# Kernel optimization log

Hardware: AMD Instinct MI355X
Metric: run time of the kernel (lower is better)

## Reference

```python
import jax, jax.numpy as jnp
import numpy as np

B, C, H, W = 4, 2048, 32, 32
HID, A, G = 512, 9, 20
SCALE = 32.0
POS_T, NEG_T = 0.7, 0.3
W_CONF, W_REG = 1.0, 5.0
EPS = 1e-8


def _anchor_base():
    # gen_anc_centers + gen_anc_base: centers at (i+0.5); anc_w=scale, anc_h=scale*ratio; clipped to feature-map extent
    scales = jnp.array([2.0, 4.0, 6.0])
    ratios = jnp.array([0.5, 1.0, 1.5])
    aw = jnp.repeat(scales, 3)                       # [A]
    ah = (scales[:, None] * ratios[None, :]).reshape(-1)
    xc = (jnp.arange(W) + 0.5)[None, :, None]        # [1,W,1]
    yc = (jnp.arange(H) + 0.5)[:, None, None]        # [H,1,1]
    x1 = jnp.clip(xc - aw / 2, 0.0, W)
    y1 = jnp.clip(yc - ah / 2, 0.0, H)
    x2 = jnp.clip(xc + aw / 2, 0.0, W)
    y2 = jnp.clip(yc + ah / 2, 0.0, H)
    anc = jnp.stack(jnp.broadcast_arrays(x1, y1, x2, y2), axis=-1)  # [H,W,A,4]
    return anc.reshape(-1, 4)                        # [N,4], N = H*W*A


def _conv(x, w, b):
    y = jax.lax.conv_general_dilated(x, w, (1, 1), 'SAME',
                                     dimension_numbers=('NCHW', 'OIHW', 'NCHW'))
    return y + b[None, :, None, None]


def setup_inputs():
    key = jax.random.key(0)
    ks = jax.random.split(key, 8)
    feature_map = jax.random.normal(ks[0], (B, C, H, W), jnp.float32)
    # valid GT boxes in pixel coords of a 1024x1024 image
    ctr = jax.random.uniform(ks[1], (B, G, 2), minval=0.15, maxval=0.85) * 1024.0
    wh = jax.random.uniform(ks[2], (B, G, 2), minval=0.05, maxval=0.30) * 1024.0
    gt_bboxes = jnp.clip(jnp.concatenate([ctr - wh / 2, ctr + wh / 2], -1), 0.0, 1024.0)
    gt_classes = jax.random.randint(ks[3], (B, G), 1, 21)
    f1 = 1.0 / np.sqrt(C * 9)
    f2 = 1.0 / np.sqrt(HID)
    conv1_w = jax.random.uniform(ks[4], (HID, C, 3, 3), jnp.float32, -f1, f1)
    conv1_b = jnp.zeros((HID,), jnp.float32)
    conf_w = jax.random.uniform(ks[5], (A, HID, 1, 1), jnp.float32, -f2, f2)
    conf_b = jnp.zeros((A,), jnp.float32)
    reg_w = jax.random.uniform(ks[6], (A * 4, HID, 1, 1), jnp.float32, -f2, f2)
    reg_b = jnp.zeros((A * 4,), jnp.float32)
    return {"feature_map": feature_map, "gt_bboxes": gt_bboxes, "gt_classes": gt_classes,
            "conv1_w": conv1_w, "conv1_b": conv1_b, "conf_w": conf_w, "conf_b": conf_b,
            "reg_w": reg_w, "reg_b": reg_b}


def reference(feature_map, gt_bboxes, gt_classes, conv1_w, conv1_b, conf_w, conf_b, reg_w, reg_b):
    # ProposalModule (dropout = eval identity)
    hid = jax.nn.relu(_conv(feature_map, conv1_w, conv1_b))
    conf = _conv(hid, conf_w, conf_b).transpose(0, 2, 3, 1).reshape(B, -1)       # [B,N]
    offs = _conv(hid, reg_w, reg_b).transpose(0, 2, 3, 1).reshape(B, -1, 4)      # [B,N,4]

    anc = _anchor_base()                              # [N,4]
    gt = gt_bboxes / SCALE                            # project_bboxes p2a

    # IoU [B,N,G]
    lt = jnp.maximum(anc[None, :, None, :2], gt[:, None, :, :2])
    rb = jnp.minimum(anc[None, :, None, 2:], gt[:, None, :, 2:])
    inter = jnp.clip(rb - lt, 0.0).prod(-1)
    area_a = (anc[:, 2] - anc[:, 0]) * (anc[:, 3] - anc[:, 1])
    area_g = (gt[..., 2] - gt[..., 0]) * (gt[..., 3] - gt[..., 1])
    iou = inter / (area_a[None, :, None] + area_g[:, None, :] - inter + EPS)

    # positive: IoU > pos_thresh OR best anchor for each GT; negative: max IoU < neg_thresh
    max_per_gt = iou.max(axis=1, keepdims=True)
    pos = ((iou > POS_T) | ((iou == max_per_gt) & (max_per_gt > EPS))).any(-1)    # [B,N]
    max_per_anc = iou.max(-1)
    gi = iou.argmax(-1)                               # assigned GT per anchor
    neg = (max_per_anc < NEG_T) & (~pos)

    assigned = jnp.take_along_axis(gt, jnp.broadcast_to(gi[:, :, None], gi.shape + (4,)), axis=1)

    acx = (anc[:, 0] + anc[:, 2]) / 2; acy = (anc[:, 1] + anc[:, 3]) / 2
    aw_ = anc[:, 2] - anc[:, 0];       ah_ = anc[:, 3] - anc[:, 1]
    gcx = (assigned[..., 0] + assigned[..., 2]) / 2; gcy = (assigned[..., 1] + assigned[..., 3]) / 2
    gw = assigned[..., 2] - assigned[..., 0];        gh = assigned[..., 3] - assigned[..., 1]
    gt_off = jnp.stack([(gcx - acx) / (aw_ + EPS), (gcy - acy) / (ah_ + EPS),
                        jnp.log((gw + EPS) / (aw_ + EPS)), jnp.log((gh + EPS) / (ah_ + EPS))], -1)

    posf = pos.astype(conf.dtype)
    negf = neg.astype(conf.dtype)
    # BCE-with-logits, reduction='sum' / batch_size (pos target 1, neg target 0)
    cls_loss = ((jax.nn.softplus(-conf) * posf).sum() + (jax.nn.softplus(conf) * negf).sum()) / B
    d = offs - gt_off
    sl1 = jnp.where(jnp.abs(d) < 1.0, 0.5 * d * d, jnp.abs(d) - 0.5)
    reg_loss = (sl1 * posf[..., None]).sum() / B
    total = W_CONF * cls_loss + W_REG * reg_loss

    # generate_proposals from positive anchors + predicted offsets (mask instead of gather for jit)
    pcx = acx + offs[..., 0] * aw_; pcy = acy + offs[..., 1] * ah_
    pw = aw_ * jnp.exp(offs[..., 2]); ph = ah_ * jnp.exp(offs[..., 3])
    proposals = jnp.stack([pcx - pw / 2, pcy - ph / 2, pcx + pw / 2, pcy + ph / 2], -1)
    proposals = proposals * posf[..., None]
    return total, proposals, pos
```

## Files before the change

kernel.cpp:

```cpp
#include <hip/hip_runtime.h>


typedef __bf16 bf16x8 __attribute__((ext_vector_type(8)));
typedef float floatx4 __attribute__((ext_vector_type(4)));

#define NB 4
#define NC 2048
#define NH 32
#define NW 32
#define NHID 512
#define NA 9
#define NG 20
#define NANC 9216
#define NM 4096

#define OFF_XH    0ull
#define OFF_WT    18939904ull
#define OFF_WH    37814272ull
#define OFF_HB    37863424ull
#define OFF_MAXG  37863680ull
#define OFF_SUMS  37864192ull
#define OFF_CTR   37864320ull
#define OFF_HIDP  37864448ull

#define PREP_TX   4096
#define PREP_W    1024
#define PREP_WH   96
#define PREP_HALO 528
#define PREP_MAXG 80
#define PREP_NBLK (PREP_TX + PREP_W + PREP_WH + PREP_HALO + PREP_MAXG + 1)

__device__ __forceinline__ unsigned short f2bf(float f) {
  unsigned int u = __float_as_uint(f);
  u = (u + 0x7fffu + ((u >> 16) & 1u)) >> 16;
  return (unsigned short)u;
}

__device__ __forceinline__ void gload16(const void* g, void* l) {
  __builtin_amdgcn_global_load_lds(
      (const __attribute__((address_space(1))) unsigned int*)g,
      (__attribute__((address_space(3))) unsigned int*)l, 16, 0, 0);
}

__constant__ float c_aw[9] = {2.f,2.f,2.f,4.f,4.f,4.f,6.f,6.f,6.f};
__constant__ float c_ah[9] = {1.f,2.f,3.f,2.f,4.f,6.f,3.f,6.f,9.f};

struct Anc { float x1, y1, x2, y2, areaA; };
__device__ __forceinline__ Anc anc_of(int n) {
  const int a = n % 9, pix = n / 9;
  const int xi = pix & 31, yi = pix >> 5;
  const float hw = c_aw[a]*0.5f, hh = c_ah[a]*0.5f;
  const float xc = xi + 0.5f, yc = yi + 0.5f;
  Anc A;
  A.x1 = fminf(fmaxf(xc - hw, 0.f), 32.f);
  A.y1 = fminf(fmaxf(yc - hh, 0.f), 32.f);
  A.x2 = fminf(fmaxf(xc + hw, 0.f), 32.f);
  A.y2 = fminf(fmaxf(yc + hh, 0.f), 32.f);
  A.areaA = __fmul_rn(__fsub_rn(A.x2, A.x1), __fsub_rn(A.y2, A.y1));
  return A;
}
__device__ __forceinline__ float iou_one(const Anc& A, float4 gp) {
  const float gx1 = gp.x * 0.03125f, gy1 = gp.y * 0.03125f;
  const float gx2 = gp.z * 0.03125f, gy2 = gp.w * 0.03125f;
  const float dx = fmaxf(__fsub_rn(fminf(A.x2, gx2), fmaxf(A.x1, gx1)), 0.f);
  const float dy = fmaxf(__fsub_rn(fminf(A.y2, gy2), fmaxf(A.y1, gy1)), 0.f);
  const float inter = __fmul_rn(dx, dy);
  const float areaG = __fmul_rn(__fsub_rn(gx2, gx1), __fsub_rn(gy2, gy1));
  const float den = __fadd_rn(__fsub_rn(__fadd_rn(A.areaA, areaG), inter), 1e-8f);
  return __fdiv_rn(inter, den);
}

__global__ __launch_bounds__(256) void k_prep(const float* __restrict__ x,
                                              const float* __restrict__ w1,
                                              const float* __restrict__ cw, const float* __restrict__ cb,
                                              const float* __restrict__ rw, const float* __restrict__ rb,
                                              const float* __restrict__ gtb,
                                              unsigned short* __restrict__ xh,
                                              unsigned short* __restrict__ wt,
                                              unsigned short* __restrict__ wh, float* __restrict__ hb,
                                              unsigned int* __restrict__ maxg,
                                              float* __restrict__ sums, unsigned int* __restrict__ ctr) {
  __shared__ float tile[64][33];
  __shared__ unsigned short wlds[9*1024];
  __shared__ float red[4];
  const int bid = blockIdx.x;
  const int tid = threadIdx.x;

  if (bid < PREP_TX) {
    const int c0 = (bid & 31) << 6;
    const int h  = (bid >> 5) & 31;
    const int b  = bid >> 10;
    const int w = tid & 31, cl = tid >> 5;
    const float* src = x + (((size_t)b*NC + c0)*NH + h)*NW;
#pragma unroll
    for (int j = 0; j < 8; ++j) {
      const int c = cl + j*8;
      tile[c][w] = src[(size_t)c*NH*NW + w];
    }
    __syncthreads();
    unsigned short* dst = xh + ((size_t)(b*34 + h + 1)*34 + 1)*2048 + c0;
    const int w2 = tid >> 3, c8 = (tid & 7) << 3;
    unsigned int pk[4];
#pragma unroll
    for (int k = 0; k < 4; ++k) {
      const unsigned int lo = f2bf(tile[c8 + 2*k][w2]);
      const unsigned int hi = f2bf(tile[c8 + 2*k + 1][w2]);
      pk[k] = lo | (hi << 16);
    }
    *(uint4*)(dst + (size_t)w2*2048 + c8) = make_uint4(pk[0], pk[1], pk[2], pk[3]);
    return;
  }
  if (bid < PREP_TX + PREP_W) {
    const int p = bid - PREP_TX;
    const int o = p >> 1, half = p & 1;
    const int c_base = half << 10;
    const float* src = w1 + ((size_t)(o*2048 + c_base))*9;
#pragma unroll
    for (int j = 0; j < 9; ++j) {
      const int f0 = (j*256 + tid)*4;
      const float4 v = *(const float4*)(src + f0);
      const float vv[4] = {v.x, v.y, v.z, v.w};
#pragma unroll
      for (int e = 0; e < 4; ++e) {
        const int f = f0 + e;
        const int c = f/9, g = f - c*9;
        wlds[g*1024 + c] = f2bf(vv[e]);
      }
    }
    __syncthreads();
#pragma unroll
    for (int j = 0; j < 5; ++j) {
      const int idx = j*256 + tid;
      if (idx < 1152) {
        const int g = idx >> 7, off = (idx & 127) << 3;
        *(uint4*)(wt + (size_t)g*NHID*NC + o*2048 + c_base + off) =
            *(const uint4*)(wlds + g*1024 + off);
      }
    }
    return;
  }
  if (bid < PREP_TX + PREP_W + PREP_WH) {
    const int t = (bid - PREP_TX - PREP_W)*256 + tid;
    const int n = t >> 9, c = t & 511;
    float v = 0.f;
    if (n < 9) v = cw[n*512 + c];
    else if (n < 45) v = rw[(n-9)*512 + c];
    wh[t] = f2bf(v);
    if (c == 0) {
      float bv = 0.f;
      if (n < 9) bv = cb[n];
      else if (n < 45) bv = rb[n-9];
      hb[n] = bv;
    }
    return;
  }
  if (bid < PREP_TX + PREP_W + PREP_WH + PREP_HALO) {
    const int q = bid - (PREP_TX + PREP_W + PREP_WH);
    const int b = q / 132, hc = q - b*132;
    int hh, ww;
    if (hc < 34)       { hh = 0;        ww = hc; }
    else if (hc < 68)  { hh = 33;       ww = hc - 34; }
    else if (hc < 100) { hh = hc - 67;  ww = 0; }
    else               { hh = hc - 99;  ww = 33; }
    uint4* dst = (uint4*)(xh + ((size_t)((b*34 + hh)*34 + ww))*2048);
    dst[tid] = make_uint4(0u, 0u, 0u, 0u);
    return;
  }
  if (bid < PREP_TX + PREP_W + PREP_WH + PREP_HALO + PREP_MAXG) {
    const int p = bid - (PREP_TX + PREP_W + PREP_WH + PREP_HALO);
    const int b = p / NG, g = p - b*NG;
    const float4 gp = *(const float4*)(gtb + ((size_t)b*NG + g)*4);
    float m = 0.f;
#pragma unroll
    for (int j = 0; j < 36; ++j)
      m = fmaxf(m, iou_one(anc_of(tid + j*256), gp));
#pragma unroll
    for (int o = 32; o > 0; o >>= 1) m = fmaxf(m, __shfl_xor(m, o));
    if ((tid & 63) == 0) red[tid >> 6] = m;
    __syncthreads();
    if (tid == 0)
      maxg[b*NG + g] = __float_as_uint(fmaxf(fmaxf(red[0], red[1]), fmaxf(red[2], red[3])));
    return;
  }
  if (tid < 2) sums[tid] = 0.f;
  else if (tid == 2) *ctr = 0u;
}

__global__ __launch_bounds__(256, 4) void k_conv_gemm(const unsigned short* __restrict__ xh,
                                                      const unsigned short* __restrict__ wt,
                                                      unsigned short* __restrict__ hidp,
                                                      int csplit, int ksh) {
  __shared__ unsigned short As[128*64] __attribute__((aligned(16)));
  __shared__ unsigned short Bs[128*64] __attribute__((aligned(16)));
  const int t = threadIdx.x;
  const int L = blockIdx.x;
  const int kz = L & ((1 << ksh) - 1);
  const int rem = L >> ksh;
  const int tileM = rem & 31, tileN = rem >> 5;
  const int b = tileM >> 3, h0 = (tileM & 7) << 2;
  const int o0 = tileN << 7;
  const int wv = t >> 6, lane = t & 63;
  const int wm = wv >> 1, wn = wv & 1;
  const int quad = lane >> 4, l16 = lane & 15;
  const int c_base = kz * csplit;

  floatx4 acc[4][4];
#pragma unroll
  for (int mt = 0; mt < 4; ++mt)
#pragma unroll
    for (int nt = 0; nt < 4; ++nt)
      acc[mt][nt] = (floatx4){0.f, 0.f, 0.f, 0.f};

  const int lr = lane >> 3, pos = lane & 7;
  int gA[4], gB[4];
#pragma unroll
  for (int j = 0; j < 4; ++j) {
    const int row = wv*32 + j*8 + lr;
    const int sd = (pos - row) & 7;
    const int hh = h0 + (row >> 5) + 1, ww = (row & 31) + 1;
    gA[j] = ((b*34 + hh)*34 + ww)*2048 + c_base + sd*8;
    gB[j] = (o0 + row)*2048 + c_base + sd*8;
  }

  for (int g = 0; g < 9; ++g) {
    const int dsp = ((g/3 - 1)*34 + (g%3 - 1)) * 2048;
    const unsigned short* wgp = wt + (size_t)g*NHID*NC;
    for (int c0 = 0; c0 < csplit; c0 += 64) {
#pragma unroll
      for (int j = 0; j < 4; ++j) {
        gload16(xh + gA[j] + dsp + c0, As + (wv*32 + j*8)*64);
        gload16(wgp + gB[j] + c0,      Bs + (wv*32 + j*8)*64);
      }
      __syncthreads();
#pragma unroll
      for (int sub = 0; sub < 2; ++sub) {
        const int ps = ((sub*4 + quad) + l16) & 7;
        bf16x8 af[4], bw[4];
#pragma unroll
        for (int mt = 0; mt < 4; ++mt)
          af[mt] = *(const bf16x8*)(As + (wm*64 + mt*16 + l16)*64 + ps*8);
#pragma unroll
        for (int nt = 0; nt < 4; ++nt)
          bw[nt] = *(const bf16x8*)(Bs + (wn*64 + nt*16 + l16)*64 + ps*8);
#pragma unroll
        for (int mt = 0; mt < 4; ++mt)
#pragma unroll
          for (int nt = 0; nt < 4; ++nt)
            acc[mt][nt] = __builtin_amdgcn_mfma_f32_16x16x32_bf16(af[mt], bw[nt], acc[mt][nt], 0, 0, 0);
      }
      __syncthreads();
    }
  }
  unsigned short* hp = hidp + (size_t)kz*NM*NHID;
#pragma unroll
  for (int mt = 0; mt < 4; ++mt) {
    const int m = tileM*128 + wm*64 + mt*16 + quad*4;
#pragma unroll
    for (int nt = 0; nt < 4; ++nt) {
      const int o = o0 + wn*64 + nt*16 + l16;
#pragma unroll
      for (int r = 0; r < 4; ++r)
        hp[(size_t)(m + r)*NHID + o] = f2bf(acc[mt][nt][r]);
    }
  }
}

__device__ __forceinline__ float softplusf(float z) {
  return fmaxf(z, 0.f) + log1pf(expf(-fabsf(z)));
}
__device__ __forceinline__ float sl1f(float d) {
  const float ad = fabsf(d);
  return ad < 1.f ? 0.5f*d*d : ad - 0.5f;
}

__global__ __launch_bounds__(256) void k_heads_assign(const unsigned short* __restrict__ hidp,
                                                      const float* __restrict__ b1,
                                                      const unsigned short* __restrict__ wh,
                                                      const float* __restrict__ hb,
                                                      const float* __restrict__ gtb,
                                                      const unsigned int* __restrict__ maxg,
                                                      float* __restrict__ out,
                                                      float* __restrict__ sums,
                                                      unsigned int* __restrict__ ctr,
                                                      int nsplit) {
  __shared__ float red[4][16][48];
  __shared__ float hl[16][49];
  __shared__ float4 gt_s[20];
  __shared__ float  mg_s[20];
  const int t = threadIdx.x;
  const int bid = blockIdx.x;
  const int b = bid >> 6, pix0 = (bid & 63) << 4;

  if (t < 20) {
    gt_s[t] = *(const float4*)(gtb + ((size_t)b*NG + t)*4);
    mg_s[t] = __uint_as_float(maxg[b*NG + t]);
  }

  const int wv = t >> 6, lane = t & 63;
  const int quad = lane >> 4, l16 = lane & 15;
  floatx4 acc[3];
#pragma unroll
  for (int nt = 0; nt < 3; ++nt) acc[nt] = (floatx4){0.f, 0.f, 0.f, 0.f};

  const int m = bid*16 + l16;
#pragma unroll
  for (int kk = 0; kk < 4; ++kk) {
    const int ch0 = wv*128 + kk*32 + quad*8;
    float s[8] = {0.f,0.f,0.f,0.f,0.f,0.f,0.f,0.f};
    const size_t gi = (size_t)m*NHID + ch0;
    for (int sp = 0; sp < nsplit; ++sp) {
      const uint4 v = *(const uint4*)(hidp + (size_t)sp*NM*NHID + gi);
      s[0] += __uint_as_float(v.x << 16); s[1] += __uint_as_float(v.x & 0xffff0000u);
      s[2] += __uint_as_float(v.y << 16); s[3] += __uint_as_float(v.y & 0xffff0000u);
      s[4] += __uint_as_float(v.z << 16); s[5] += __uint_as_float(v.z & 0xffff0000u);
      s[6] += __uint_as_float(v.w << 16); s[7] += __uint_as_float(v.w & 0xffff0000u);
    }
    union { unsigned short u[8]; bf16x8 v; } af;
#pragma unroll
    for (int e = 0; e < 8; ++e)
      af.u[e] = f2bf(fmaxf(s[e] + b1[ch0 + e], 0.f));
#pragma unroll
    for (int nt = 0; nt < 3; ++nt) {
      const bf16x8 bf = *(const bf16x8*)(wh + (size_t)(nt*16 + l16)*NHID + ch0);
      acc[nt] = __builtin_amdgcn_mfma_f32_16x16x32_bf16(af.v, bf, acc[nt], 0, 0, 0);
    }
  }
#pragma unroll
  for (int nt = 0; nt < 3; ++nt)
#pragma unroll
    for (int r = 0; r < 4; ++r)
      red[wv][quad*4 + r][nt*16 + l16] = acc[nt][r];
  __syncthreads();
#pragma unroll
  for (int j = 0; j < 3; ++j) {
    const int idx = t + j*256;
    const int i = idx / 48, c = idx - i*48;
    hl[i][c] = red[0][i][c] + red[1][i][c] + red[2][i][c] + red[3][i][c] + hb[c];
  }
  __syncthreads();

  float cs = 0.f, rs = 0.f;
  if (t < 144) {
    const int pixL = t / 9, a = t - pixL*9;
    const int pix = pix0 + pixL;
    const int n = pix*9 + a;
    const int idx = b*NANC + n;
    const Anc A = anc_of(n);

    float mx = -1.f; int gi = 0; bool pos = false;
    for (int g = 0; g < NG; ++g) {
      const float v = iou_one(A, gt_s[g]);
      const float mg = mg_s[g];
      pos = pos || (v > 0.7f) || ((v == mg) && (mg > 1e-8f));
      if (v > mx) { mx = v; gi = g; }
    }
    const bool neg = (mx < 0.3f) && !pos;
    const float posf = pos ? 1.f : 0.f;

    const float conf = hl[pixL][a];
    const float of0 = hl[pixL][9 + a*4 + 0];
    const float of1 = hl[pixL][9 + a*4 + 1];
    const float of2 = hl[pixL][9 + a*4 + 2];
    const float of3 = hl[pixL][9 + a*4 + 3];

    if (pos) cs = softplusf(-conf);
    else if (neg) cs = softplusf(conf);

    const float acx = (A.x1 + A.x2)*0.5f, acy = (A.y1 + A.y2)*0.5f;
    const float aw = A.x2 - A.x1, ah = A.y2 - A.y1;
    if (pos) {
      const float4 gp = gt_s[gi];
      const float gx1 = gp.x*0.03125f, gy1 = gp.y*0.03125f;
      const float gx2 = gp.z*0.03125f, gy2 = gp.w*0.03125f;
      const float gcx = (gx1+gx2)*0.5f, gcy = (gy1+gy2)*0.5f;
      const float gw = gx2-gx1, gh = gy2-gy1;
      const float t0 = (gcx-acx)/(aw+1e-8f), t1 = (gcy-acy)/(ah+1e-8f);
      const float t2 = logf((gw+1e-8f)/(aw+1e-8f)), t3 = logf((gh+1e-8f)/(ah+1e-8f));
      rs = sl1f(of0-t0) + sl1f(of1-t1) + sl1f(of2-t2) + sl1f(of3-t3);
    }

    const float pcx = acx + of0*aw, pcy = acy + of1*ah;
    const float pw = aw*expf(of2), ph = ah*expf(of3);
    float* op = out + 1 + (size_t)idx*4;
    op[0] = (pcx - pw*0.5f)*posf;
    op[1] = (pcy - ph*0.5f)*posf;
    op[2] = (pcx + pw*0.5f)*posf;
    op[3] = (pcy + ph*0.5f)*posf;
    out[1 + 4*(size_t)NB*NANC + idx] = posf;
  }
#pragma unroll
  for (int o = 32; o > 0; o >>= 1) { cs += __shfl_xor(cs, o); rs += __shfl_xor(rs, o); }
  if ((t & 63) == 0) { atomicAdd(&sums[0], cs); atomicAdd(&sums[1], rs); }

  __syncthreads();
  if (t == 0) {
    __threadfence();
    const unsigned int c = atomicAdd(ctr, 1u);
    if (c == 255u) {
      __threadfence();
      const float fcs = atomicAdd(&sums[0], 0.f);
      const float frs = atomicAdd(&sums[1], 0.f);
      out[0] = fcs*0.25f + 5.f*(frs*0.25f);
    }
  }
}

extern "C" void kernel_launch(void* const* d_in, const int* in_sizes, int n_in,
                              void* d_out, int out_size, void* d_ws, size_t ws_size,
                              hipStream_t stream) {
  const float* x   = (const float*)d_in[0];
  const float* gtb = (const float*)d_in[1];
  const float* w1  = (const float*)d_in[3];
  const float* b1  = (const float*)d_in[4];
  const float* cw  = (const float*)d_in[5];
  const float* cb  = (const float*)d_in[6];
  const float* rw  = (const float*)d_in[7];
  const float* rb  = (const float*)d_in[8];
  float* out = (float*)d_out;
  char* ws = (char*)d_ws;

  unsigned short* xh    = (unsigned short*)(ws + OFF_XH);
  unsigned short* wt    = (unsigned short*)(ws + OFF_WT);
  unsigned short* wh    = (unsigned short*)(ws + OFF_WH);
  float*          hb    = (float*)(ws + OFF_HB);
  unsigned int*   maxg  = (unsigned int*)(ws + OFF_MAXG);
  float*          sums  = (float*)(ws + OFF_SUMS);
  unsigned int*   ctr   = (unsigned int*)(ws + OFF_CTR);
  unsigned short* hidp  = (unsigned short*)(ws + OFF_HIDP);

  int nsplit = 8, ksh = 3;
  while (nsplit > 1 && OFF_HIDP + (size_t)nsplit*NM*NHID*2 > ws_size) { nsplit >>= 1; --ksh; }
  const int csplit = NC / nsplit;

  k_prep<<<PREP_NBLK, 256, 0, stream>>>(x, w1, cw, cb, rw, rb, gtb, xh, wt, wh, hb, maxg, sums, ctr);
  k_conv_gemm<<<128*nsplit, 256, 0, stream>>>(xh, wt, hidp, csplit, ksh);
  k_heads_assign<<<256, 256, 0, stream>>>(hidp, b1, wh, hb, gtb, maxg, out, sums, ctr, nsplit);
}
```

Baseline: 230.1 us.

## Enlarge conv GEMM tiles to 256x256 with double-buffered LDS prefetch

The implicit-GEMM conv kernel moves from 128x128 tiles with 4 waves to 256x256 tiles with 8 waves, each wave computing 128x64. The 3x3 tap and channel loops are flattened into one k-loop, and global-to-LDS loads are double-buffered with explicit vmcnt waits and raw barriers so the next tile's loads overlap the current MFMAs. This is meant to raise arithmetic intensity and hide load latency. In exchange it uses 128KB of LDS and more accumulator registers per block, and launches four times fewer blocks, which lowers occupancy and may underfill the CUs.

```diff
diff --git a/kernel.cpp b/kernel.cpp
--- a/kernel.cpp
+++ b/kernel.cpp
@@ -44,6 +44,7 @@
 
 __constant__ float c_aw[9] = {2.f,2.f,2.f,4.f,4.f,4.f,6.f,6.f,6.f};
 __constant__ float c_ah[9] = {1.f,2.f,3.f,2.f,4.f,6.f,3.f,6.f,9.f};
+__constant__ int c_dsp[9] = {-71680, -69632, -67584, -2048, 0, 2048, 67584, 69632, 71680};
 
 struct Anc { float x1, y1, x2, y2, areaA; };
 __device__ __forceinline__ Anc anc_of(int n) {
@@ -186,27 +187,34 @@
   else if (tid == 2) *ctr = 0u;
 }
 
-__global__ __launch_bounds__(256, 4) void k_conv_gemm(const unsigned short* __restrict__ xh,
-                                                      const unsigned short* __restrict__ wt,
-                                                      unsigned short* __restrict__ hidp,
-                                                      int csplit, int ksh) {
-  __shared__ unsigned short As[128*64] __attribute__((aligned(16)));
-  __shared__ unsigned short Bs[128*64] __attribute__((aligned(16)));
+__device__ __forceinline__ void wgbar() {
+  asm volatile("" ::: "memory");
+  __builtin_amdgcn_s_barrier();
+  asm volatile("" ::: "memory");
+}
+
+__global__ __launch_bounds__(512) void k_conv_gemm(const unsigned short* __restrict__ xh,
+                                                   const unsigned short* __restrict__ wt,
+                                                   unsigned short* __restrict__ hidp,
+                                                   int csplit, int ksh) {
+  __shared__ unsigned short As[2][256*64] __attribute__((aligned(16)));
+  __shared__ unsigned short Bs[2][256*64] __attribute__((aligned(16)));
   const int t = threadIdx.x;
   const int L = blockIdx.x;
   const int kz = L & ((1 << ksh) - 1);
-  const int rem = L >> ksh;
-  const int tileM = rem & 31, tileN = rem >> 5;
-  const int b = tileM >> 3, h0 = (tileM & 7) << 2;
-  const int o0 = tileN << 7;
+  const int tile = L >> ksh;
+  const int tileM = tile & 15, tileN = tile >> 4;
+  const int o0 = tileN << 8;
   const int wv = t >> 6, lane = t & 63;
-  const int wm = wv >> 1, wn = wv & 1;
+  const int wm = wv >> 2, wn = wv & 3;
   const int quad = lane >> 4, l16 = lane & 15;
   const int c_base = kz * csplit;
-
-  floatx4 acc[4][4];
-#pragma unroll
-  for (int mt = 0; mt < 4; ++mt)
+  const int tpg = csplit >> 6;
+  const int NT = 9 * tpg;
+
+  floatx4 acc[8][4];
+#pragma unroll
+  for (int mt = 0; mt < 8; ++mt)
 #pragma unroll
     for (int nt = 0; nt < 4; ++nt)
       acc[mt][nt] = (floatx4){0.f, 0.f, 0.f, 0.f};
@@ -215,49 +223,75 @@
   int gA[4], gB[4];
 #pragma unroll
   for (int j = 0; j < 4; ++j) {
-    const int row = wv*32 + j*8 + lr;
-    const int sd = (pos - row) & 7;
-    const int hh = h0 + (row >> 5) + 1, ww = (row & 31) + 1;
+    const int r = j*64 + wv*8 + lr;
+    const int sd = (pos - r) & 7;
+    const int pix = tileM*256 + r;
+    const int b = pix >> 10;
+    const int hh = ((pix >> 5) & 31) + 1, ww = (pix & 31) + 1;
     gA[j] = ((b*34 + hh)*34 + ww)*2048 + c_base + sd*8;
-    gB[j] = (o0 + row)*2048 + c_base + sd*8;
-  }
-
-  for (int g = 0; g < 9; ++g) {
-    const int dsp = ((g/3 - 1)*34 + (g%3 - 1)) * 2048;
-    const unsigned short* wgp = wt + (size_t)g*NHID*NC;
-    for (int c0 = 0; c0 < csplit; c0 += 64) {
-#pragma unroll
-      for (int j = 0; j < 4; ++j) {
-        gload16(xh + gA[j] + dsp + c0, As + (wv*32 + j*8)*64);
-        gload16(wgp + gB[j] + c0,      Bs + (wv*32 + j*8)*64);
-      }
-      __syncthreads();
-#pragma unroll
-      for (int sub = 0; sub < 2; ++sub) {
-        const int ps = ((sub*4 + quad) + l16) & 7;
-        bf16x8 af[4], bw[4];
-#pragma unroll
-        for (int mt = 0; mt < 4; ++mt)
-          af[mt] = *(const bf16x8*)(As + (wm*64 + mt*16 + l16)*64 + ps*8);
+    gB[j] = (o0 + r)*2048 + c_base + sd*8;
+  }
+
+  {
+    const int dsp = c_dsp[0];
+#pragma unroll
+    for (int j = 0; j < 4; ++j)
+      gload16(xh + gA[j] + dsp, &As[0][(j*64 + wv*8)*64]);
+#pragma unroll
+    for (int j = 0; j < 4; ++j)
+      gload16(wt + gB[j], &Bs[0][(j*64 + wv*8)*64]);
+  }
+
+  int gq = 0, cq = 0, buf = 0;
+  for (int kt = 0; kt < NT; ++kt) {
+    int ng = gq, ncq = cq + 1;
+    if (ncq == tpg) { ncq = 0; ++ng; }
+    if (kt + 1 < NT) {
+      const int dsp = c_dsp[ng], co = ncq << 6;
+      const size_t wgo = (size_t)ng * NHID * NC;
+#pragma unroll
+      for (int j = 0; j < 4; ++j)
+        gload16(xh + gA[j] + dsp + co, &As[buf^1][(j*64 + wv*8)*64]);
+#pragma unroll
+      for (int j = 0; j < 4; ++j)
+        gload16(wt + wgo + gB[j] + co, &Bs[buf^1][(j*64 + wv*8)*64]);
+      asm volatile("s_waitcnt vmcnt(8)" ::: "memory");
+    } else {
+      asm volatile("s_waitcnt vmcnt(0)" ::: "memory");
+    }
+    wgbar();
+
+    const unsigned short* Asb = As[buf];
+    const unsigned short* Bsb = Bs[buf];
+#pragma unroll
+    for (int sub = 0; sub < 2; ++sub) {
+      const int ps = ((sub*4 + quad) + l16) & 7;
+      bf16x8 af[8], bw[4];
+#pragma unroll
+      for (int mt = 0; mt < 8; ++mt)
+        af[mt] = *(const bf16x8*)(Asb + (wm*128 + mt*16 + l16)*64 + ps*8);
+#pragma unroll
+      for (int nt = 0; nt < 4; ++nt)
+        bw[nt] = *(const bf16x8*)(Bsb + (wn*64 + nt*16 + l16)*64 + ps*8);
+#pragma unroll
+      for (int mt = 0; mt < 8; ++mt)
 #pragma unroll
         for (int nt = 0; nt < 4; ++nt)
-          bw[nt] = *(const bf16x8*)(Bs + (wn*64 + nt*16 + l16)*64 + ps*8);
-#pragma unroll
-        for (int mt = 0; mt < 4; ++mt)
-#pragma unroll
-          for (int nt = 0; nt < 4; ++nt)
-            acc[mt][nt] = __builtin_amdgcn_mfma_f32_16x16x32_bf16(af[mt], bw[nt], acc[mt][nt], 0, 0, 0);
-      }
-      __syncthreads();
-    }
-  }
+          acc[mt][nt] = __builtin_amdgcn_mfma_f32_16x16x32_bf16(af[mt], bw[nt], acc[mt][nt], 0, 0, 0);
+    }
+    wgbar();
+    gq = ng; cq = ncq; buf ^= 1;
+  }
+
   unsigned short* hp = hidp + (size_t)kz*NM*NHID;
-#pragma unroll
-  for (int mt = 0; mt < 4; ++mt) {
-    const int m = tileM*128 + wm*64 + mt*16 + quad*4;
+  const int m0 = tileM*256 + wm*128;
+  const int oc = o0 + wn*64;
+#pragma unroll
+  for (int mt = 0; mt < 8; ++mt) {
+    const int m = m0 + mt*16 + quad*4;
 #pragma unroll
     for (int nt = 0; nt < 4; ++nt) {
-      const int o = o0 + wn*64 + nt*16 + l16;
+      const int o = oc + nt*16 + l16;
 #pragma unroll
       for (int r = 0; r < 4; ++r)
         hp[(size_t)(m + r)*NHID + o] = f2bf(acc[mt][nt][r]);
@@ -433,6 +467,6 @@
   const int csplit = NC / nsplit;
 
   k_prep<<<PREP_NBLK, 256, 0, stream>>>(x, w1, cw, cb, rw, rb, gtb, xh, wt, wh, hb, maxg, sums, ctr);
-  k_conv_gemm<<<128*nsplit, 256, 0, stream>>>(xh, wt, hidp, csplit, ksh);
+  k_conv_gemm<<<32*nsplit, 512, 0, stream>>>(xh, wt, hidp, csplit, ksh);
   k_heads_assign<<<256, 256, 0, stream>>>(hidp, b1, wh, hb, gtb, maxg, out, sums, ctr, nsplit);
 }
```

Measured after the change: 231.8 us. About the same (+0.7%).
